# Kernel tuning notes

Hardware: AMD Instinct MI355X
Metric: run time of the kernel (lower is better)

Reference implementation:

```python
import jax, jax.numpy as jnp
import numpy as np

WS = 7        # window_size
SHIFT = 3     # shift_size
NH = 3        # num_heads
E = 96        # embed_dim
B, H, W = 8, 224, 224


def _relative_position_index(ws: int) -> np.ndarray:
    coords = np.stack(np.meshgrid(np.arange(ws), np.arange(ws), indexing='ij')).reshape(2, -1)
    rel = coords[:, :, None] - coords[:, None, :]          # (2, N, N)
    rel = rel.transpose(1, 2, 0) + (ws - 1)                # (N, N, 2)
    rel[:, :, 0] *= 2 * ws - 1
    return rel.sum(-1)                                      # (N, N) in [0, (2ws-1)^2)


def setup_inputs() -> dict:
    key = jax.random.key(0)
    ks = jax.random.split(key, 6)
    x = jax.random.normal(ks[0], (B, H, W, E), dtype=jnp.float32)
    # nn.MultiheadAttention params: packed in_proj (3E,E)+(3E,), out_proj (E,E)+(E,)
    w_qkv = jax.random.normal(ks[1], (3 * E, E), dtype=jnp.float32) * 0.02
    b_qkv = jax.random.normal(ks[2], (3 * E,), dtype=jnp.float32) * 0.02
    w_out = jax.random.normal(ks[3], (E, E), dtype=jnp.float32) * 0.02
    b_out = jax.random.normal(ks[4], (E,), dtype=jnp.float32) * 0.02
    bias_table = jax.random.normal(ks[5], ((2 * WS - 1) ** 2, NH), dtype=jnp.float32) * 0.02
    rel_index = jnp.asarray(_relative_position_index(WS), dtype=jnp.int32)
    return {"x": x, "w_qkv": w_qkv, "b_qkv": b_qkv, "w_out": w_out,
            "b_out": b_out, "bias_table": bias_table, "rel_index": rel_index}


def reference(x, w_qkv, b_qkv, w_out, b_out, bias_table, rel_index):
    ws, shift = WS, SHIFT
    Bq, Hq, Wq, C = x.shape
    nh = bias_table.shape[-1]
    hd = C // nh
    N = ws * ws

    # cyclic shift
    xs = jnp.roll(x, (-shift, -shift), axis=(1, 2))

    Hp = -(-Hq // ws) * ws
    Wp = -(-Wq // ws) * ws
    xs = jnp.pad(xs, ((0, 0), (0, Hp - Hq), (0, Wp - Wq), (0, 0)))

    # window partition -> (B*nW, N, C)
    win = xs.reshape(Bq, Hp // ws, ws, Wp // ws, ws, C)
    win = win.transpose(0, 1, 3, 2, 4, 5).reshape(-1, N, C)

    # packed QKV projection (torch Linear: x @ W.T + b)
    qkv = win @ w_qkv.T + b_qkv
    q, k, v = jnp.split(qkv, 3, axis=-1)
    hsplit = lambda t: t.reshape(t.shape[0], N, nh, hd)
    q, k, v = hsplit(q), hsplit(k), hsplit(v)

    # scaled attention scores + relative position bias (used as attn_mask in torch)
    scale = 1.0 / jnp.sqrt(jnp.asarray(hd, dtype=q.dtype))
    scores = jnp.einsum('bnhd,bmhd->bhnm', q * scale, k)    # (B*nW, h, N, N)
    bias = bias_table[rel_index].transpose(2, 0, 1)         # (h, N, N)
    attn = jax.nn.softmax(scores + bias[None], axis=-1)

    out = jnp.einsum('bhnm,bmhd->bnhd', attn, v).reshape(-1, N, C)
    out = out @ w_out.T + b_out

    # window reverse + crop + reverse shift
    out = out.reshape(Bq, Hp // ws, Wp // ws, ws, ws, C)
    out = out.transpose(0, 1, 3, 2, 4, 5).reshape(Bq, Hp, Wp, C)[:, :Hq, :Wq, :]
    return jnp.roll(out, (shift, shift), axis=(1, 2))
```

## Files before the change

kernel.cpp:

```cpp
#include <hip/hip_runtime.h>
#include <cstddef>


typedef _Float16 half8 __attribute__((ext_vector_type(8)));
typedef float f4v __attribute__((ext_vector_type(4)));
typedef unsigned short u16;
typedef unsigned int u32;

#define MFMA(A, B, C) __builtin_amdgcn_mfma_f32_16x16x32_f16((A), (B), (C), 0, 0, 0)

__device__ inline u16 f16b(float f) { return __builtin_bit_cast(u16, (_Float16)f); }
__device__ inline u32 pk2(float a, float b) {
    return (u32)__builtin_bit_cast(u16, (_Float16)a) |
           ((u32)__builtin_bit_cast(u16, (_Float16)b) << 16);
}

__global__ void prep_kernel(const float* __restrict__ wqkv, const float* __restrict__ wout,
                            const float* __restrict__ btab, const int* __restrict__ ridx,
                            u16* __restrict__ wq16, u16* __restrict__ wo16,
                            float* __restrict__ bmat)
{
    const int i = blockIdx.x * 256 + threadIdx.x;
    if (i < 27648) {
        wq16[i] = f16b(wqkv[i]);
    } else if (i < 36864) {
        wo16[i - 27648] = f16b(wout[i - 27648]);
    } else if (i < 36864 + 9408) {
        const int j = i - 36864;
        const int h = j / 3136, rem = j - h * 3136;
        const int r = rem >> 6, u = rem & 63;
        bmat[j] = (u < 49) ? btab[ridx[r * 49 + u] * 3 + h] : 0.f;
    }
}

__global__ __launch_bounds__(512, 6)
void swin_kernel(const float* __restrict__ x,
                 const u16* __restrict__ wq16,
                 const u16* __restrict__ wo16,
                 const float* __restrict__ bqkv,
                 const float* __restrict__ bout,
                 const float* __restrict__ bm,
                 float* __restrict__ out)
{
    __shared__ __attribute__((aligned(16))) char smem[53584];
    u16* qt  = (u16*)smem;
    u16* kt  = (u16*)(smem + 12288);
    u16* pt  = (u16*)smem;
    u16* vt  = (u16*)(smem + 24576);
    u16* sc  = (u16*)(smem + 36864);
    u16* aot = (u16*)(smem + 36864);
    u32* pix = (u32*)(smem + 53328);

    const int tid  = threadIdx.x;
    const int w    = tid >> 6;
    const int lane = tid & 63;
    const int l15  = lane & 15;
    const int lg   = lane >> 4;

    const int blk = blockIdx.x;
    const int bb  = blk >> 10;
    const int wi7 = ((blk >> 5) & 31) * 7;
    const int wj7 = (blk & 31) * 7;

    if (tid < 64) {
        const int t = tid;
        const int tr = t / 7, tc = t - tr * 7;
        int r = wi7 + tr + 3; if (r >= 224) r -= 224;
        int c = wj7 + tc + 3; if (c >= 224) c -= 224;
        pix[t] = (u32)(((bb * 224 + r) * 224 + c) * 96);
    }

    {
        const int mh2 = (w >> 2) * 2;
        half8 a[2][3];
        #pragma unroll
        for (int mi = 0; mi < 2; ++mi) {
            const int t = (mh2 + mi) * 16 + l15;
            if (t < 49) {
                const int tr = t / 7, tc = t - tr * 7;
                int r = wi7 + tr + 3; if (r >= 224) r -= 224;
                int c = wj7 + tc + 3; if (c >= 224) c -= 224;
                const float* xrow = x + ((size_t)((bb * 224 + r) * 224 + c)) * 96 + lg * 8;
                #pragma unroll
                for (int ks = 0; ks < 3; ++ks) {
                    const float4 f0 = *(const float4*)(xrow + ks * 32);
                    const float4 f1 = *(const float4*)(xrow + ks * 32 + 4);
                    half8 hv;
                    hv[0] = (_Float16)f0.x; hv[1] = (_Float16)f0.y;
                    hv[2] = (_Float16)f0.z; hv[3] = (_Float16)f0.w;
                    hv[4] = (_Float16)f1.x; hv[5] = (_Float16)f1.y;
                    hv[6] = (_Float16)f1.z; hv[7] = (_Float16)f1.w;
                    a[mi][ks] = hv;
                }
            } else {
                const half8 hz = {0, 0, 0, 0, 0, 0, 0, 0};
                a[mi][0] = hz; a[mi][1] = hz; a[mi][2] = hz;
            }
        }
        const int nw = w & 3;
        for (int n = nw; n < 18; n += 4) {
            const u16* bp = wq16 + (size_t)(n * 16 + l15) * 96 + lg * 8;
            const half8 b0 = *(const half8*)(bp);
            const half8 b1 = *(const half8*)(bp + 32);
            const half8 b2 = *(const half8*)(bp + 64);
            f4v acc0 = {0.f, 0.f, 0.f, 0.f}, acc1 = {0.f, 0.f, 0.f, 0.f};
            acc0 = MFMA(a[0][0], b0, acc0);
            acc0 = MFMA(a[0][1], b1, acc0);
            acc0 = MFMA(a[0][2], b2, acc0);
            acc1 = MFMA(a[1][0], b0, acc1);
            acc1 = MFMA(a[1][1], b1, acc1);
            acc1 = MFMA(a[1][2], b2, acc1);
            const int oc = n * 16 + l15;
            const float bias = bqkv[oc];
            if (n < 12) {
                const int c  = (n < 6) ? oc : oc - 96;
                const int hh = c >> 5, d = c & 31;
                u16* dst = (n < 6) ? qt : kt;
                const float mul = (n < 6) ? 0.17677669529663688f : 1.0f;
                const int eb = ((d >> 3) * 16) * 8 + (d & 7);
                #pragma unroll
                for (int mi = 0; mi < 2; ++mi) {
                    const int mt = mh2 + mi;
                    const int fb = (hh * 4 + mt) * 512 + eb;
                    #pragma unroll
                    for (int i = 0; i < 4; ++i) {
                        const float v = ((mi ? acc1[i] : acc0[i]) + bias) * mul;
                        dst[fb + (lg * 4 + i) * 8] = f16b(v);
                    }
                }
            } else {
                const int c  = oc - 192;
                const int hh = c >> 5, ndt = (c >> 4) & 1, dcol = c & 15;
                #pragma unroll
                for (int mi = 0; mi < 2; ++mi) {
                    const int mt = mh2 + mi;
                    #pragma unroll
                    for (int i = 0; i < 4; ++i) {
                        const int u = mt * 16 + lg * 4 + i;
                        const float v = (mi ? acc1[i] : acc0[i]) + bias;
                        vt[((hh * 2 + ndt) * 2 + (u >> 5)) * 512 +
                           (((u & 31) >> 3) * 16 + dcol) * 8 + (u & 7)] = f16b(v);
                    }
                }
            }
        }
    }
    __syncthreads();

    {
        const int ut = w & 3;
        const int pbase = (w >> 2) * 6;
        const int u = ut * 16 + l15;
        const bool colok = u < 56;
        #pragma unroll
        for (int q6 = 0; q6 < 6; ++q6) {
            const int p = pbase + q6, h = p >> 2, m = p & 3;
            const half8 qa = *(const half8*)&qt[(h * 4 + m) * 512 + lane * 8];
            const half8 kb = *(const half8*)&kt[(h * 4 + ut) * 512 + lane * 8];
            f4v z = {0.f, 0.f, 0.f, 0.f};
            const f4v s = MFMA(qa, kb, z);
            #pragma unroll
            for (int i = 0; i < 4; ++i) {
                const int t = m * 16 + lg * 4 + i;
                if (t < 49 && colok)
                    sc[(h * 49 + t) * 56 + u] = f16b(s[i]);
            }
        }
    }
    __syncthreads();

    {
        const int sub = tid & 3;
        const int u0 = sub * 16;
        for (int rr = tid >> 2; rr < 147; rr += 128) {
            const int h = (rr >= 98) ? 2 : (rr >= 49 ? 1 : 0);
            const int t = rr - h * 49;
            const u16* srow = sc + (h * 49 + t) * 56 + u0;
            const float* brow = bm + (h * 49 + t) * 64 + u0;
            float vals[16];
            float mx = -1e30f;
            #pragma unroll
            for (int g = 0; g < 2; ++g) {
                const half8 sv = *(const half8*)(srow + g * 8);
                const float4 bv0 = *(const float4*)(brow + g * 8);
                const float4 bv1 = *(const float4*)(brow + g * 8 + 4);
                const float bArr[8] = {bv0.x, bv0.y, bv0.z, bv0.w, bv1.x, bv1.y, bv1.z, bv1.w};
                #pragma unroll
                for (int j = 0; j < 8; ++j) {
                    const int u = u0 + g * 8 + j;
                    const float v = (u < 49) ? ((float)sv[j] + bArr[j]) : -1e30f;
                    vals[g * 8 + j] = v;
                    mx = fmaxf(mx, v);
                }
            }
            mx = fmaxf(mx, __shfl_xor(mx, 1));
            mx = fmaxf(mx, __shfl_xor(mx, 2));
            float sm = 0.f;
            #pragma unroll
            for (int j = 0; j < 16; ++j) { const float e = __expf(vals[j] - mx); vals[j] = e; sm += e; }
            sm += __shfl_xor(sm, 1);
            sm += __shfl_xor(sm, 2);
            const float inv = 1.f / sm;
            #pragma unroll
            for (int j = 0; j < 16; ++j) vals[j] *= inv;
            const int base = h * 4096 + ((t >> 4) * 2 + (u0 >> 5)) * 512 +
                             ((t & 15) + 16 * ((u0 & 31) >> 3)) * 8;
            uint4 w0, w1;
            w0.x = pk2(vals[0],  vals[1]);  w0.y = pk2(vals[2],  vals[3]);
            w0.z = pk2(vals[4],  vals[5]);  w0.w = pk2(vals[6],  vals[7]);
            w1.x = pk2(vals[8],  vals[9]);  w1.y = pk2(vals[10], vals[11]);
            w1.z = pk2(vals[12], vals[13]); w1.w = pk2(vals[14], vals[15]);
            *(uint4*)&pt[base] = w0;
            *(uint4*)&pt[base + 128] = w1;
        }
    }
    __syncthreads();

    {
        const int nd = (w >> 2) & 1;
        const int m  = w & 3;
        const int kl = nd * 16 + l15;
        const int abase = ((kl >> 3) * 16) * 8 + (kl & 7);
        #pragma unroll
        for (int h = 0; h < 3; ++h) {
            f4v acc = {0.f, 0.f, 0.f, 0.f};
            #pragma unroll
            for (int ku = 0; ku < 2; ++ku) {
                const half8 pa = *(const half8*)&pt[h * 4096 + (m * 2 + ku) * 512 + lane * 8];
                const half8 vb = *(const half8*)&vt[((h * 2 + nd) * 2 + ku) * 512 + lane * 8];
                acc = MFMA(pa, vb, acc);
            }
            const int fb = (m * 3 + h) * 512 + abase;
            #pragma unroll
            for (int i = 0; i < 4; ++i)
                aot[fb + (lg * 4 + i) * 8] = f16b(acc[i]);
        }
    }
    __syncthreads();

    {
        #pragma unroll
        for (int q3 = 0; q3 < 3; ++q3) {
            const int p = q3 * 8 + w;
            const int n = p >> 2, m = p & 3;
            const u16* bp = wo16 + (size_t)(n * 16 + l15) * 96 + lg * 8;
            const half8 b0 = *(const half8*)(bp);
            const half8 b1 = *(const half8*)(bp + 32);
            const half8 b2 = *(const half8*)(bp + 64);
            f4v acc = {0.f, 0.f, 0.f, 0.f};
            acc = MFMA(*(const half8*)&aot[(m * 3 + 0) * 512 + lane * 8], b0, acc);
            acc = MFMA(*(const half8*)&aot[(m * 3 + 1) * 512 + lane * 8], b1, acc);
            acc = MFMA(*(const half8*)&aot[(m * 3 + 2) * 512 + lane * 8], b2, acc);
            const float bo = bout[n * 16 + l15];
            #pragma unroll
            for (int i = 0; i < 4; ++i) {
                const int t = m * 16 + lg * 4 + i;
                if (t < 49)
                    out[(size_t)pix[t] + n * 16 + l15] = acc[i] + bo;
            }
        }
    }
}

extern "C" void kernel_launch(void* const* d_in, const int* in_sizes, int n_in,
                              void* d_out, int out_size, void* d_ws, size_t ws_size,
                              hipStream_t stream) {
    const float* x          = (const float*)d_in[0];
    const float* w_qkv      = (const float*)d_in[1];
    const float* b_qkv      = (const float*)d_in[2];
    const float* w_out      = (const float*)d_in[3];
    const float* b_out      = (const float*)d_in[4];
    const float* bias_table = (const float*)d_in[5];
    const int*   rel_index  = (const int*)d_in[6];
    float* outp = (float*)d_out;

    u16* wq16 = (u16*)d_ws;
    u16* wo16 = wq16 + 27648;
    float* bmat = (float*)((char*)d_ws + 73728);

    prep_kernel<<<dim3(181), dim3(256), 0, stream>>>(
        w_qkv, w_out, bias_table, rel_index, wq16, wo16, bmat);
    swin_kernel<<<dim3(8192), dim3(512), 0, stream>>>(
        x, wq16, wo16, b_qkv, b_out, bmat, outp);
}
```

Measured before the change: 229.1 us.

## Restructure swin window kernel: 4 waves, fused in-register softmax, swizzled LDS, vector stores

The window kernel drops to 256 threads with each wave owning a 16-row query tile. QK^T, bias add, softmax and PV now run in registers per wave, so the score buffer in LDS and two block barriers are gone. Shared-memory tiles use an XOR swizzle to reduce bank conflicts, and fp16 conversion uses packed cvt_pkrtz. QKV weight loads are double-buffered, and the output projection is transposed so results go out as float4 stores. In exchange each wave does more work and holds more registers, which may lower occupancy, and rounding changes to round-toward-zero.

```diff
diff --git a/kernel.cpp b/kernel.cpp
--- a/kernel.cpp
+++ b/kernel.cpp
@@ -10,9 +10,11 @@
 #define MFMA(A, B, C) __builtin_amdgcn_mfma_f32_16x16x32_f16((A), (B), (C), 0, 0, 0)
 
 __device__ inline u16 f16b(float f) { return __builtin_bit_cast(u16, (_Float16)f); }
-__device__ inline u32 pk2(float a, float b) {
-    return (u32)__builtin_bit_cast(u16, (_Float16)a) |
-           ((u32)__builtin_bit_cast(u16, (_Float16)b) << 16);
+__device__ inline u32 pkrtz(float a, float b) {
+    return __builtin_bit_cast(u32, __builtin_amdgcn_cvt_pkrtz(a, b));
+}
+__device__ inline int SWU(int a, int kg) {
+    return (((a ^ (kg << 1) ^ ((a & 8) >> 1)) & 15) | (kg << 4));
 }
 
 __global__ void prep_kernel(const float* __restrict__ wqkv, const float* __restrict__ wout,
@@ -25,15 +27,15 @@
         wq16[i] = f16b(wqkv[i]);
     } else if (i < 36864) {
         wo16[i - 27648] = f16b(wout[i - 27648]);
-    } else if (i < 36864 + 9408) {
+    } else if (i < 36864 + 12288) {
         const int j = i - 36864;
-        const int h = j / 3136, rem = j - h * 3136;
+        const int h = j >> 12, rem = j & 4095;
         const int r = rem >> 6, u = rem & 63;
-        bmat[j] = (u < 49) ? btab[ridx[r * 49 + u] * 3 + h] : 0.f;
-    }
-}
-
-__global__ __launch_bounds__(512, 6)
+        bmat[j] = (r < 49 && u < 49) ? btab[ridx[r * 49 + u] * 3 + h] : 0.f;
+    }
+}
+
+__global__ __launch_bounds__(256, 4)
 void swin_kernel(const float* __restrict__ x,
                  const u16* __restrict__ wq16,
                  const u16* __restrict__ wo16,
@@ -42,14 +44,8 @@
                  const float* __restrict__ bm,
                  float* __restrict__ out)
 {
-    __shared__ __attribute__((aligned(16))) char smem[53584];
-    u16* qt  = (u16*)smem;
-    u16* kt  = (u16*)(smem + 12288);
-    u16* pt  = (u16*)smem;
-    u16* vt  = (u16*)(smem + 24576);
-    u16* sc  = (u16*)(smem + 36864);
-    u16* aot = (u16*)(smem + 36864);
-    u32* pix = (u32*)(smem + 53328);
+    __shared__ __attribute__((aligned(16))) char smem[40960];
+    constexpr int QT = 0, KT = 12288, VT = 24576, PL = 36864;
 
     const int tid  = threadIdx.x;
     const int w    = tid >> 6;
@@ -62,201 +58,184 @@
     const int wi7 = ((blk >> 5) & 31) * 7;
     const int wj7 = (blk & 31) * 7;
 
-    if (tid < 64) {
-        const int t = tid;
-        const int tr = t / 7, tc = t - tr * 7;
-        int r = wi7 + tr + 3; if (r >= 224) r -= 224;
-        int c = wj7 + tc + 3; if (c >= 224) c -= 224;
-        pix[t] = (u32)(((bb * 224 + r) * 224 + c) * 96);
+    const float SCALE = 0.17677669529663688f;
+    const int swbase = SWU(l15, lg) * 16;
+
+    half8 xa[4][3];
+    #pragma unroll
+    for (int m = 0; m < 4; ++m) {
+        const int t = m * 16 + l15;
+        if (t < 49) {
+            const int tr = t / 7, tc = t - tr * 7;
+            int r = wi7 + tr + 3; if (r >= 224) r -= 224;
+            int c = wj7 + tc + 3; if (c >= 224) c -= 224;
+            const float* xrow = x + ((size_t)((bb * 224 + r) * 224 + c)) * 96 + lg * 8;
+            #pragma unroll
+            for (int ks = 0; ks < 3; ++ks) {
+                const float4 f0 = *(const float4*)(xrow + ks * 32);
+                const float4 f1 = *(const float4*)(xrow + ks * 32 + 4);
+                uint4 pk;
+                pk.x = pkrtz(f0.x, f0.y); pk.y = pkrtz(f0.z, f0.w);
+                pk.z = pkrtz(f1.x, f1.y); pk.w = pkrtz(f1.z, f1.w);
+                xa[m][ks] = __builtin_bit_cast(half8, pk);
+            }
+        } else {
+            const uint4 z = {0, 0, 0, 0};
+            xa[m][0] = xa[m][1] = xa[m][2] = __builtin_bit_cast(half8, z);
+        }
     }
 
     {
-        const int mh2 = (w >> 2) * 2;
-        half8 a[2][3];
-        #pragma unroll
-        for (int mi = 0; mi < 2; ++mi) {
-            const int t = (mh2 + mi) * 16 + l15;
-            if (t < 49) {
-                const int tr = t / 7, tc = t - tr * 7;
-                int r = wi7 + tr + 3; if (r >= 224) r -= 224;
-                int c = wj7 + tc + 3; if (c >= 224) c -= 224;
-                const float* xrow = x + ((size_t)((bb * 224 + r) * 224 + c)) * 96 + lg * 8;
-                #pragma unroll
-                for (int ks = 0; ks < 3; ++ks) {
-                    const float4 f0 = *(const float4*)(xrow + ks * 32);
-                    const float4 f1 = *(const float4*)(xrow + ks * 32 + 4);
-                    half8 hv;
-                    hv[0] = (_Float16)f0.x; hv[1] = (_Float16)f0.y;
-                    hv[2] = (_Float16)f0.z; hv[3] = (_Float16)f0.w;
-                    hv[4] = (_Float16)f1.x; hv[5] = (_Float16)f1.y;
-                    hv[6] = (_Float16)f1.z; hv[7] = (_Float16)f1.w;
-                    a[mi][ks] = hv;
-                }
-            } else {
-                const half8 hz = {0, 0, 0, 0, 0, 0, 0, 0};
-                a[mi][0] = hz; a[mi][1] = hz; a[mi][2] = hz;
-            }
-        }
-        const int nw = w & 3;
-        for (int n = nw; n < 18; n += 4) {
+        const int sw1 = ((lg >> 1) & 1) * 4;
+        half8 bcur[3], bnxt[3];
+        int n = w;
+        {
             const u16* bp = wq16 + (size_t)(n * 16 + l15) * 96 + lg * 8;
-            const half8 b0 = *(const half8*)(bp);
-            const half8 b1 = *(const half8*)(bp + 32);
-            const half8 b2 = *(const half8*)(bp + 64);
-            f4v acc0 = {0.f, 0.f, 0.f, 0.f}, acc1 = {0.f, 0.f, 0.f, 0.f};
-            acc0 = MFMA(a[0][0], b0, acc0);
-            acc0 = MFMA(a[0][1], b1, acc0);
-            acc0 = MFMA(a[0][2], b2, acc0);
-            acc1 = MFMA(a[1][0], b0, acc1);
-            acc1 = MFMA(a[1][1], b1, acc1);
-            acc1 = MFMA(a[1][2], b2, acc1);
+            bcur[0] = *(const half8*)(bp);
+            bcur[1] = *(const half8*)(bp + 32);
+            bcur[2] = *(const half8*)(bp + 64);
+        }
+        while (true) {
+            const int n2 = n + 4;
+            if (n2 < 18) {
+                const u16* bp = wq16 + (size_t)(n2 * 16 + l15) * 96 + lg * 8;
+                bnxt[0] = *(const half8*)(bp);
+                bnxt[1] = *(const half8*)(bp + 32);
+                bnxt[2] = *(const half8*)(bp + 64);
+            }
+            f4v acc[4];
+            #pragma unroll
+            for (int m = 0; m < 4; ++m) {
+                f4v a = {0.f, 0.f, 0.f, 0.f};
+                a = MFMA(xa[m][0], bcur[0], a);
+                a = MFMA(xa[m][1], bcur[1], a);
+                a = MFMA(xa[m][2], bcur[2], a);
+                acc[m] = a;
+            }
             const int oc = n * 16 + l15;
             const float bias = bqkv[oc];
             if (n < 12) {
                 const int c  = (n < 6) ? oc : oc - 96;
                 const int hh = c >> 5, d = c & 31;
-                u16* dst = (n < 6) ? qt : kt;
-                const float mul = (n < 6) ? 0.17677669529663688f : 1.0f;
-                const int eb = ((d >> 3) * 16) * 8 + (d & 7);
-                #pragma unroll
-                for (int mi = 0; mi < 2; ++mi) {
-                    const int mt = mh2 + mi;
-                    const int fb = (hh * 4 + mt) * 512 + eb;
+                const int kg = d >> 3, el = d & 7;
+                const float mul = (n < 6) ? SCALE : 1.0f;
+                char* reg0 = smem + ((n < 6) ? QT : KT) + (hh * 4) * 1024 + el * 2;
+                const int xr = (kg << 1) ^ sw1;
+                #pragma unroll
+                for (int m = 0; m < 4; ++m) {
                     #pragma unroll
                     for (int i = 0; i < 4; ++i) {
-                        const float v = ((mi ? acc1[i] : acc0[i]) + bias) * mul;
-                        dst[fb + (lg * 4 + i) * 8] = f16b(v);
+                        const float v = (acc[m][i] + bias) * mul;
+                        const int unit = (((lg * 4 + i) ^ xr) & 15) | (kg << 4);
+                        *(u16*)(reg0 + m * 1024 + unit * 16) = f16b(v);
                     }
                 }
             } else {
                 const int c  = oc - 192;
-                const int hh = c >> 5, ndt = (c >> 4) & 1, dcol = c & 15;
-                #pragma unroll
-                for (int mi = 0; mi < 2; ++mi) {
-                    const int mt = mh2 + mi;
-                    #pragma unroll
-                    for (int i = 0; i < 4; ++i) {
-                        const int u = mt * 16 + lg * 4 + i;
-                        const float v = (mi ? acc1[i] : acc0[i]) + bias;
-                        vt[((hh * 2 + ndt) * 2 + (u >> 5)) * 512 +
-                           (((u & 31) >> 3) * 16 + dcol) * 8 + (u & 7)] = f16b(v);
-                    }
+                const int hh = c >> 5, nd = (c >> 4) & 1;
+                const int elb = (lg & 1) * 4;
+                #pragma unroll
+                for (int m = 0; m < 4; ++m) {
+                    const int ku = m >> 1;
+                    const int kg = (m & 1) * 2 + (lg >> 1);
+                    uint2 pv;
+                    pv.x = pkrtz(acc[m][0] + bias, acc[m][1] + bias);
+                    pv.y = pkrtz(acc[m][2] + bias, acc[m][3] + bias);
+                    *(uint2*)(smem + VT + ((hh * 2 + nd) * 2 + ku) * 1024 +
+                              SWU(l15, kg) * 16 + elb * 2) = pv;
                 }
             }
+            if (n2 >= 18) break;
+            bcur[0] = bnxt[0]; bcur[1] = bnxt[1]; bcur[2] = bnxt[2];
+            n = n2;
         }
     }
     __syncthreads();
 
     {
-        const int ut = w & 3;
-        const int pbase = (w >> 2) * 6;
-        const int u = ut * 16 + l15;
-        const bool colok = u < 56;
-        #pragma unroll
-        for (int q6 = 0; q6 < 6; ++q6) {
-            const int p = pbase + q6, h = p >> 2, m = p & 3;
-            const half8 qa = *(const half8*)&qt[(h * 4 + m) * 512 + lane * 8];
-            const half8 kb = *(const half8*)&kt[(h * 4 + ut) * 512 + lane * 8];
-            f4v z = {0.f, 0.f, 0.f, 0.f};
-            const f4v s = MFMA(qa, kb, z);
-            #pragma unroll
-            for (int i = 0; i < 4; ++i) {
-                const int t = m * 16 + lg * 4 + i;
-                if (t < 49 && colok)
-                    sc[(h * 49 + t) * 56 + u] = f16b(s[i]);
-            }
-        }
-    }
-    __syncthreads();
-
-    {
-        const int sub = tid & 3;
-        const int u0 = sub * 16;
-        for (int rr = tid >> 2; rr < 147; rr += 128) {
-            const int h = (rr >= 98) ? 2 : (rr >= 49 ? 1 : 0);
-            const int t = rr - h * 49;
-            const u16* srow = sc + (h * 49 + t) * 56 + u0;
-            const float* brow = bm + (h * 49 + t) * 64 + u0;
-            float vals[16];
+        const int t = w * 16 + l15;
+        const int elb2 = ((lg & 1) * 4) * 2;
+        for (int h = 0; h < 3; ++h) {
+            const int qfr = QT + (h * 4 + w) * 1024;
+            const half8 qa = *(const half8*)(smem + qfr + swbase);
+            f4v s[4];
+            #pragma unroll
+            for (int ut = 0; ut < 4; ++ut) {
+                const half8 kb = *(const half8*)(smem + KT + (h * 4 + ut) * 1024 + swbase);
+                f4v z = {0.f, 0.f, 0.f, 0.f};
+                s[ut] = MFMA(kb, qa, z);
+            }
+            const float* bp = bm + h * 4096 + t * 64 + lg * 4;
+            #pragma unroll
+            for (int ut = 0; ut < 4; ++ut) {
+                const float4 bv = *(const float4*)(bp + ut * 16);
+                s[ut][0] += bv.x; s[ut][1] += bv.y; s[ut][2] += bv.z; s[ut][3] += bv.w;
+            }
+            s[3][1] = -1e30f; s[3][2] = -1e30f; s[3][3] = -1e30f;
+            if (lg) s[3][0] = -1e30f;
             float mx = -1e30f;
             #pragma unroll
-            for (int g = 0; g < 2; ++g) {
-                const half8 sv = *(const half8*)(srow + g * 8);
-                const float4 bv0 = *(const float4*)(brow + g * 8);
-                const float4 bv1 = *(const float4*)(brow + g * 8 + 4);
-                const float bArr[8] = {bv0.x, bv0.y, bv0.z, bv0.w, bv1.x, bv1.y, bv1.z, bv1.w};
-                #pragma unroll
-                for (int j = 0; j < 8; ++j) {
-                    const int u = u0 + g * 8 + j;
-                    const float v = (u < 49) ? ((float)sv[j] + bArr[j]) : -1e30f;
-                    vals[g * 8 + j] = v;
-                    mx = fmaxf(mx, v);
-                }
-            }
-            mx = fmaxf(mx, __shfl_xor(mx, 1));
-            mx = fmaxf(mx, __shfl_xor(mx, 2));
+            for (int ut = 0; ut < 4; ++ut)
+                #pragma unroll
+                for (int i = 0; i < 4; ++i) mx = fmaxf(mx, s[ut][i]);
+            mx = fmaxf(mx, __shfl_xor(mx, 16));
+            mx = fmaxf(mx, __shfl_xor(mx, 32));
             float sm = 0.f;
             #pragma unroll
-            for (int j = 0; j < 16; ++j) { const float e = __expf(vals[j] - mx); vals[j] = e; sm += e; }
-            sm += __shfl_xor(sm, 1);
-            sm += __shfl_xor(sm, 2);
+            for (int ut = 0; ut < 4; ++ut)
+                #pragma unroll
+                for (int i = 0; i < 4; ++i) { const float e = __expf(s[ut][i] - mx); s[ut][i] = e; sm += e; }
+            sm += __shfl_xor(sm, 16);
+            sm += __shfl_xor(sm, 32);
             const float inv = 1.f / sm;
             #pragma unroll
-            for (int j = 0; j < 16; ++j) vals[j] *= inv;
-            const int base = h * 4096 + ((t >> 4) * 2 + (u0 >> 5)) * 512 +
-                             ((t & 15) + 16 * ((u0 & 31) >> 3)) * 8;
-            uint4 w0, w1;
-            w0.x = pk2(vals[0],  vals[1]);  w0.y = pk2(vals[2],  vals[3]);
-            w0.z = pk2(vals[4],  vals[5]);  w0.w = pk2(vals[6],  vals[7]);
-            w1.x = pk2(vals[8],  vals[9]);  w1.y = pk2(vals[10], vals[11]);
-            w1.z = pk2(vals[12], vals[13]); w1.w = pk2(vals[14], vals[15]);
-            *(uint4*)&pt[base] = w0;
-            *(uint4*)&pt[base + 128] = w1;
-        }
-    }
-    __syncthreads();
-
-    {
-        const int nd = (w >> 2) & 1;
-        const int m  = w & 3;
-        const int kl = nd * 16 + l15;
-        const int abase = ((kl >> 3) * 16) * 8 + (kl & 7);
-        #pragma unroll
-        for (int h = 0; h < 3; ++h) {
-            f4v acc = {0.f, 0.f, 0.f, 0.f};
-            #pragma unroll
-            for (int ku = 0; ku < 2; ++ku) {
-                const half8 pa = *(const half8*)&pt[h * 4096 + (m * 2 + ku) * 512 + lane * 8];
-                const half8 vb = *(const half8*)&vt[((h * 2 + nd) * 2 + ku) * 512 + lane * 8];
-                acc = MFMA(pa, vb, acc);
-            }
-            const int fb = (m * 3 + h) * 512 + abase;
-            #pragma unroll
-            for (int i = 0; i < 4; ++i)
-                aot[fb + (lg * 4 + i) * 8] = f16b(acc[i]);
+            for (int ut = 0; ut < 4; ++ut) {
+                uint2 pv;
+                pv.x = pkrtz(s[ut][0] * inv, s[ut][1] * inv);
+                pv.y = pkrtz(s[ut][2] * inv, s[ut][3] * inv);
+                const int kg = (ut & 1) * 2 + (lg >> 1);
+                const int base = (ut < 2) ? qfr : (PL + w * 1024);
+                *(uint2*)(smem + base + SWU(l15, kg) * 16 + elb2) = pv;
+            }
+            const half8 p0 = *(const half8*)(smem + qfr + swbase);
+            const half8 p1 = *(const half8*)(smem + PL + w * 1024 + swbase);
+            #pragma unroll
+            for (int nd = 0; nd < 2; ++nd) {
+                f4v o = {0.f, 0.f, 0.f, 0.f};
+                o = MFMA(*(const half8*)(smem + VT + ((h * 2 + nd) * 2 + 0) * 1024 + swbase), p0, o);
+                o = MFMA(*(const half8*)(smem + VT + ((h * 2 + nd) * 2 + 1) * 1024 + swbase), p1, o);
+                uint2 ov;
+                ov.x = pkrtz(o[0], o[1]);
+                ov.y = pkrtz(o[2], o[3]);
+                const int kg = nd * 2 + (lg >> 1);
+                *(uint2*)(smem + qfr + SWU(l15, kg) * 16 + elb2) = ov;
+            }
         }
     }
     __syncthreads();
 
     {
         #pragma unroll
-        for (int q3 = 0; q3 < 3; ++q3) {
-            const int p = q3 * 8 + w;
-            const int n = p >> 2, m = p & 3;
-            const u16* bp = wo16 + (size_t)(n * 16 + l15) * 96 + lg * 8;
-            const half8 b0 = *(const half8*)(bp);
-            const half8 b1 = *(const half8*)(bp + 32);
-            const half8 b2 = *(const half8*)(bp + 64);
+        for (int q = 0; q < 6; ++q) {
+            const int p = w * 6 + q;
+            const int nn = p >> 2, m = p & 3;
             f4v acc = {0.f, 0.f, 0.f, 0.f};
-            acc = MFMA(*(const half8*)&aot[(m * 3 + 0) * 512 + lane * 8], b0, acc);
-            acc = MFMA(*(const half8*)&aot[(m * 3 + 1) * 512 + lane * 8], b1, acc);
-            acc = MFMA(*(const half8*)&aot[(m * 3 + 2) * 512 + lane * 8], b2, acc);
-            const float bo = bout[n * 16 + l15];
-            #pragma unroll
-            for (int i = 0; i < 4; ++i) {
-                const int t = m * 16 + lg * 4 + i;
-                if (t < 49)
-                    out[(size_t)pix[t] + n * 16 + l15] = acc[i] + bo;
+            #pragma unroll
+            for (int ks = 0; ks < 3; ++ks) {
+                const half8 wa = *(const half8*)(wo16 + (size_t)(nn * 16 + l15) * 96 + ks * 32 + lg * 8);
+                const half8 ob = *(const half8*)(smem + QT + (ks * 4 + m) * 1024 + swbase);
+                acc = MFMA(wa, ob, acc);
+            }
+            const int t = m * 16 + l15;
+            if (t < 49) {
+                const int tr = t / 7, tc = t - tr * 7;
+                int r = wi7 + tr + 3; if (r >= 224) r -= 224;
+                int c = wj7 + tc + 3; if (c >= 224) c -= 224;
+                const float4 bo = *(const float4*)(bout + nn * 16 + lg * 4);
+                float4 res;
+                res.x = acc[0] + bo.x; res.y = acc[1] + bo.y;
+                res.z = acc[2] + bo.z; res.w = acc[3] + bo.w;
+                *(float4*)(out + ((size_t)((bb * 224 + r) * 224 + c)) * 96 + nn * 16 + lg * 4) = res;
             }
         }
     }
@@ -278,8 +257,8 @@
     u16* wo16 = wq16 + 27648;
     float* bmat = (float*)((char*)d_ws + 73728);
 
-    prep_kernel<<<dim3(181), dim3(256), 0, stream>>>(
+    prep_kernel<<<dim3(192), dim3(256), 0, stream>>>(
         w_qkv, w_out, bias_table, rel_index, wq16, wo16, bmat);
-    swin_kernel<<<dim3(8192), dim3(512), 0, stream>>>(
+    swin_kernel<<<dim3(8192), dim3(256), 0, stream>>>(
         x, wq16, wo16, b_qkv, b_out, bmat, outp);
 }
```

New measurement: 201.7 us. -12.0%, faster.
